# Optimization experiments

Hardware: AMD Instinct MI355X
Metric: run time of the kernel (lower is better)

Reference implementation:

```python
import jax, jax.numpy as jnp
import numpy as np

HEAD_SIZE = 64


def setup_inputs() -> dict:
    key = jax.random.key(0)
    kx, kk, kq, kv = jax.random.split(key, 4)
    B, T, C = 4, 4096, 1024
    x = jax.random.normal(kx, (B, T, C), dtype=jnp.float32)
    Wk = jax.random.normal(kk, (C, HEAD_SIZE), dtype=jnp.float32) * 0.02
    Wq = jax.random.normal(kq, (C, HEAD_SIZE), dtype=jnp.float32) * 0.02
    Wv = jax.random.normal(kv, (C, HEAD_SIZE), dtype=jnp.float32) * 0.02
    return {"x": x, "Wk": Wk, "Wq": Wq, "Wv": Wv}


def reference(x, Wk, Wq, Wv):
    # x: (B,T,C); projections to (B,T,H)
    T = x.shape[1]
    k = jnp.einsum('btc,ch->bth', x, Wk)
    q = jnp.einsum('btc,ch->bth', x, Wq)
    v = jnp.einsum('btc,ch->bth', x, Wv)
    scale = 1.0 / jnp.sqrt(jnp.float32(HEAD_SIZE))
    wei = jnp.einsum('bth,bsh->bts', q, k) * scale  # (B,T,T)
    causal = jnp.tril(jnp.ones((T, T), dtype=bool))
    wei = jnp.where(causal, wei, -jnp.inf)
    wei = jax.nn.softmax(wei, axis=-1)
    out = jnp.einsum('bts,bsh->bth', wei, v)  # (B,T,H)
    return out
```

## Files before the change

kernel.cpp:

```cpp
#include <hip/hip_runtime.h>

typedef __attribute__((ext_vector_type(8))) short short8;
typedef __attribute__((ext_vector_type(4))) float f32x4;
typedef unsigned short u16;

#define BB 4
#define TT 4096
#define CC 1024
#define HH 64

static __device__ __forceinline__ u16 f2bf(float f) {
    unsigned int u = __float_as_uint(f);
    unsigned int r = (u + 0x7FFFu + ((u >> 16) & 1u)) >> 16;
    return (u16)r;
}

static __device__ __forceinline__ unsigned int cvtpk(float lo, float hi) {
    unsigned int r;
    asm("v_cvt_pk_bf16_f32 %0, %1, %2" : "=v"(r) : "v"(lo), "v"(hi));
    return r;
}

static __device__ __forceinline__ int swz(int row, int chunk) {
    return row * 64 + ((chunk ^ (row & 7)) << 3);
}

static __device__ __forceinline__ int probe_isbf(const u16* xu, int tid) {
    int lane = tid & 63;
    int cnt = 0;
    for (int i = lane; i < 1024; i += 64) {
        u16 u = xu[2 * i];
        int e = (u >> 7) & 0xFF;
        cnt += (e >= 100 && e <= 140) ? 1 : 0;
    }
    for (int d = 1; d < 64; d <<= 1) cnt += __shfl_xor(cnt, d);
    return (cnt > 512) ? 1 : 0;
}

__global__ void prep(const void* __restrict__ Wk, const void* __restrict__ Wq,
                     const void* __restrict__ Wv, const u16* __restrict__ xu,
                     u16* __restrict__ Wtp, int* __restrict__ flag) {
    __shared__ int sflag;
    if (threadIdx.x < 64) {
        int f = probe_isbf(xu, threadIdx.x);
        if (threadIdx.x == 0) sflag = f;
    }
    __syncthreads();
    const int isbf = sflag;

    if (blockIdx.x >= 192) {
        if (threadIdx.x == 0) *flag = isbf;
        return;
    }

    int r = blockIdx.x;
    int p = r >> 6;
    int n = r & 63;
    int nt = n >> 4, nl = n & 15;
    const void* W = (p == 0) ? Wq : (p == 1) ? Wk : Wv;
    int k0 = threadIdx.x * 4;
    int kb = k0 >> 6, k2 = (k0 >> 5) & 1, quad = (k0 >> 3) & 3, half = (k0 >> 2) & 1;
    ushort4 v;
    if (isbf) {
        const u16* Wb = (const u16*)W;
        v.x = Wb[(k0 + 0) * HH + n]; v.y = Wb[(k0 + 1) * HH + n];
        v.z = Wb[(k0 + 2) * HH + n]; v.w = Wb[(k0 + 3) * HH + n];
    } else {
        const float* Wf = (const float*)W;
        v.x = f2bf(Wf[(k0 + 0) * HH + n]); v.y = f2bf(Wf[(k0 + 1) * HH + n]);
        v.z = f2bf(Wf[(k0 + 2) * HH + n]); v.w = f2bf(Wf[(k0 + 3) * HH + n]);
    }
    size_t off16 = ((size_t)((p * 4 + nt) * 16 + kb) * 2 + k2) * 64 + quad * 16 + nl;
    *reinterpret_cast<ushort4*>(Wtp + off16 * 8 + half * 4) = v;
}

__global__ __launch_bounds__(256) void qkv_proj(const void* __restrict__ x,
                                                const u16* __restrict__ Wtp,
                                                u16* __restrict__ qo, u16* __restrict__ ko,
                                                u16* __restrict__ vo, const int* __restrict__ flag) {
    __shared__ __align__(16) u16 xs[32 * 1024];
    __shared__ __align__(16) u16 tls[4][3][256];
    const int isbf = *flag;
    const int tid = threadIdx.x;
    const int lane = tid & 63;
    const int w = tid >> 6;
    const int l15 = lane & 15;
    const int quad = lane >> 4;
    int phys = blockIdx.x;
    int rb = (phys & 7) * 64 + (phys >> 3);
    const int g0r = rb * 32;

    #pragma unroll
    for (int j = 0; j < 16; j++) {
        int c = tid + j * 256;
        int row = c >> 7, ck = c & 127;
        int dst = row * 1024 + ((ck ^ (row & 7)) << 3);
        if (isbf) {
            uint4 d = *reinterpret_cast<const uint4*>((const u16*)x + (size_t)(g0r + row) * CC + ck * 8);
            *reinterpret_cast<uint4*>(xs + dst) = d;
        } else {
            const float4* pf = reinterpret_cast<const float4*>((const float*)x + (size_t)(g0r + row) * CC + ck * 8);
            float4 a0 = pf[0], a1 = pf[1];
            ushort4 lo; lo.x = f2bf(a0.x); lo.y = f2bf(a0.y); lo.z = f2bf(a0.z); lo.w = f2bf(a0.w);
            ushort4 hi; hi.x = f2bf(a1.x); hi.y = f2bf(a1.y); hi.z = f2bf(a1.z); hi.w = f2bf(a1.w);
            *reinterpret_cast<ushort4*>(xs + dst) = lo;
            *reinterpret_cast<ushort4*>(xs + dst + 4) = hi;
        }
    }
    __syncthreads();

    f32x4 zero = {0.f, 0.f, 0.f, 0.f};
    f32x4 acc[3][2];
    #pragma unroll
    for (int i = 0; i < 3; i++) { acc[i][0] = zero; acc[i][1] = zero; }

    for (int kb = 0; kb < 16; kb++) {
        #pragma unroll
        for (int k2 = 0; k2 < 2; k2++) {
            int ck = kb * 8 + k2 * 4 + quad;
            int xo = ((ck ^ (l15 & 7)) << 3);
            short8 af0 = *reinterpret_cast<const short8*>(xs + l15 * 1024 + xo);
            short8 af1 = *reinterpret_cast<const short8*>(xs + (16 + l15) * 1024 + xo);
            #pragma unroll
            for (int p = 0; p < 3; p++) {
                short8 bf = *reinterpret_cast<const short8*>(
                    Wtp + ((((size_t)(p * 4 + w) * 16 + kb) * 2 + k2) * 64 + lane) * 8);
                acc[p][0] = __builtin_amdgcn_mfma_f32_16x16x32_bf16(af0, bf, acc[p][0], 0, 0, 0);
                acc[p][1] = __builtin_amdgcn_mfma_f32_16x16x32_bf16(af1, bf, acc[p][1], 0, 0, 0);
            }
        }
    }

    const float qscale = 0.18033688011112042f;
    #pragma unroll
    for (int rt = 0; rt < 2; rt++) {
        const int g0rt = g0r + rt * 16;
        #pragma unroll
        for (int p = 0; p < 3; p++) {
            if (p < 2) {
                float sc = (p == 0) ? qscale : 1.f;
                #pragma unroll
                for (int r = 0; r < 4; r++)
                    tls[w][p][(quad * 4 + r) * 16 + l15] = f2bf(acc[p][rt][r] * sc);
            } else {
                #pragma unroll
                for (int r = 0; r < 4; r++)
                    tls[w][p][l15 * 16 + quad * 4 + r] = f2bf(acc[p][rt][r]);
            }
        }
        #pragma unroll
        for (int p = 0; p < 2; p++) {
            int t = lane >> 2, seg = lane & 3;
            ushort4 d = *reinterpret_cast<const ushort4*>(&tls[w][p][t * 16 + seg * 4]);
            u16* dst = (p == 0) ? qo : ko;
            *reinterpret_cast<ushort4*>(dst + (size_t)(g0rt + t) * HH + w * 16 + seg * 4) = d;
        }
        {
            int c = lane >> 2, seg = lane & 3;
            ushort4 d = *reinterpret_cast<const ushort4*>(&tls[w][2][c * 16 + seg * 4]);
            int b = g0rt >> 12;
            int kt = (g0rt & 4095) >> 6;
            int toff = g0rt & 63;
            *reinterpret_cast<ushort4*>(vo + ((size_t)((b * 64 + kt) * 64 + w * 16 + c)) * 64 + toff + seg * 4) = d;
        }
    }
}

__global__ __launch_bounds__(256) void attn(const u16* __restrict__ qp, const u16* __restrict__ kp,
                                            const u16* __restrict__ vp, float* __restrict__ acco,
                                            float* __restrict__ accl, void* __restrict__ outv,
                                            const int* __restrict__ flag, int nsplit) {
    __shared__ __align__(16) u16 kst[64 * 64];
    __shared__ __align__(16) u16 vts[64 * 64];
    __shared__ __align__(16) u16 pb[4][16 * 64];
    const int isbf = *flag;
    const int tid = threadIdx.x;
    const int lane = tid & 63;
    const int w = tid >> 6;
    const int l15 = lane & 15;
    const int quad = lane >> 4;

    int u = blockIdx.x;
    int b, qt, ks;
    if (nsplit == 1) {
        b = u >> 6;
        int raw = u & 63;
        qt = (raw & 1) ? (63 - (raw >> 1)) : (raw >> 1);
        ks = 0;
    } else {
        int per = 64 * nsplit;
        b = u / per;
        int rem = u - b * per;
        int i = rem / nsplit;
        qt = 63 - i;
        ks = rem - i * nsplit;
    }
    int qbase = qt * 64;
    int diag = qt;
    int nkt = diag + 1;
    if (ks >= nkt) return;

    const int q_g = qbase + w * 16 + l15;

    short8 aq[2];
    {
        const u16* qrow = qp + (size_t)(b * TT + q_g) * HH;
        aq[0] = *reinterpret_cast<const short8*>(qrow + quad * 8);
        aq[1] = *reinterpret_cast<const short8*>(qrow + 32 + quad * 8);
    }

    const int cc0 = tid, cc1 = tid + 256;
    const int dst0 = swz(cc0 >> 3, cc0 & 7);
    const int dst1 = swz(cc1 >> 3, cc1 & 7);
    const u16* kbase = kp + (size_t)b * TT * HH;
    const u16* vbase = vp + (size_t)b * 64 * 64 * 64;

    f32x4 zero = {0.f, 0.f, 0.f, 0.f};
    f32x4 o[4];
    #pragma unroll
    for (int i = 0; i < 4; i++) o[i] = zero;
    float lsum = 0.f;

    uint4 rk0 = *reinterpret_cast<const uint4*>(kbase + (size_t)ks * 4096 + cc0 * 8);
    uint4 rk1 = *reinterpret_cast<const uint4*>(kbase + (size_t)ks * 4096 + cc1 * 8);
    uint4 rv0 = *reinterpret_cast<const uint4*>(vbase + (size_t)ks * 4096 + cc0 * 8);
    uint4 rv1 = *reinterpret_cast<const uint4*>(vbase + (size_t)ks * 4096 + cc1 * 8);

    for (int kt = ks; kt < nkt; kt += nsplit) {
        __syncthreads();
        *reinterpret_cast<uint4*>(&kst[dst0]) = rk0;
        *reinterpret_cast<uint4*>(&kst[dst1]) = rk1;
        *reinterpret_cast<uint4*>(&vts[dst0]) = rv0;
        *reinterpret_cast<uint4*>(&vts[dst1]) = rv1;
        __syncthreads();
        int ktn = kt + nsplit;
        if (ktn < nkt) {
            rk0 = *reinterpret_cast<const uint4*>(kbase + (size_t)ktn * 4096 + cc0 * 8);
            rk1 = *reinterpret_cast<const uint4*>(kbase + (size_t)ktn * 4096 + cc1 * 8);
            rv0 = *reinterpret_cast<const uint4*>(vbase + (size_t)ktn * 4096 + cc0 * 8);
            rv1 = *reinterpret_cast<const uint4*>(vbase + (size_t)ktn * 4096 + cc1 * 8);
        }
        f32x4 s[4];
        #pragma unroll
        for (int i = 0; i < 4; i++) s[i] = zero;
        __builtin_amdgcn_s_setprio(1);
        #pragma unroll
        for (int k2 = 0; k2 < 2; k2++) {
            #pragma unroll
            for (int nt = 0; nt < 4; nt++) {
                short8 af = *reinterpret_cast<const short8*>(&kst[swz(nt * 16 + l15, k2 * 4 + quad)]);
                s[nt] = __builtin_amdgcn_mfma_f32_16x16x32_bf16(af, aq[k2], s[nt], 0, 0, 0);
            }
        }
        __builtin_amdgcn_s_setprio(0);
        const bool dm = (kt == diag);
        #pragma unroll
        for (int nt = 0; nt < 4; nt++) {
            int key0 = kt * 64 + nt * 16 + quad * 4;
            #pragma unroll
            for (int r = 0; r < 4; r++) {
                float p = __builtin_amdgcn_exp2f(s[nt][r]);
                if (dm && key0 + r > q_g) p = 0.f;
                s[nt][r] = p;
            }
        }
        #pragma unroll
        for (int nt = 0; nt < 4; nt++)
            lsum += (s[nt][0] + s[nt][1]) + (s[nt][2] + s[nt][3]);
        #pragma unroll
        for (int nt = 0; nt < 4; nt++) {
            uint2 pk;
            pk.x = cvtpk(s[nt][0], s[nt][1]);
            pk.y = cvtpk(s[nt][2], s[nt][3]);
            int addr = swz(l15, nt * 2 + (quad >> 1)) + (quad & 1) * 4;
            *reinterpret_cast<uint2*>(&pb[w][addr]) = pk;
        }
        __builtin_amdgcn_s_setprio(1);
        #pragma unroll
        for (int k2 = 0; k2 < 2; k2++) {
            short8 bp = *reinterpret_cast<const short8*>(&pb[w][swz(l15, k2 * 4 + quad)]);
            #pragma unroll
            for (int nt = 0; nt < 4; nt++) {
                short8 av = *reinterpret_cast<const short8*>(&vts[swz(nt * 16 + l15, k2 * 4 + quad)]);
                o[nt] = __builtin_amdgcn_mfma_f32_16x16x32_bf16(av, bp, o[nt], 0, 0, 0);
            }
        }
        __builtin_amdgcn_s_setprio(0);
    }

    lsum += __shfl_xor(lsum, 16);
    lsum += __shfl_xor(lsum, 32);

    const size_t g0q = (size_t)(b * TT) + q_g;

    if (nsplit == 1) {
        float inv = 1.0f / lsum;
        if (isbf) {
            u16* outp = (u16*)outv;
            #pragma unroll
            for (int nt = 0; nt < 4; nt++) {
                ushort4 sv;
                sv.x = f2bf(o[nt][0] * inv); sv.y = f2bf(o[nt][1] * inv);
                sv.z = f2bf(o[nt][2] * inv); sv.w = f2bf(o[nt][3] * inv);
                *reinterpret_cast<ushort4*>(outp + g0q * HH + nt * 16 + quad * 4) = sv;
            }
        } else {
            float* outp = (float*)outv;
            #pragma unroll
            for (int nt = 0; nt < 4; nt++) {
                float4 sv = {o[nt][0] * inv, o[nt][1] * inv, o[nt][2] * inv, o[nt][3] * inv};
                *reinterpret_cast<float4*>(outp + g0q * HH + nt * 16 + quad * 4) = sv;
            }
        }
    } else {
        float* accos = acco + (size_t)ks * (BB * TT * HH);
        float* accls = accl + (size_t)ks * (BB * TT);
        #pragma unroll
        for (int nt = 0; nt < 4; nt++) {
            float4 sv = {o[nt][0], o[nt][1], o[nt][2], o[nt][3]};
            *reinterpret_cast<float4*>(accos + g0q * HH + nt * 16 + quad * 4) = sv;
        }
        if (quad == 0) accls[g0q] = lsum;
    }
}

__global__ __launch_bounds__(256) void attn_finalize(const float* __restrict__ acco,
                                                     const float* __restrict__ accl,
                                                     void* __restrict__ outv,
                                                     const int* __restrict__ flag, int nsplit) {
    const int isbf = *flag;
    int i = blockIdx.x * blockDim.x + threadIdx.x;
    int row = i >> 4;
    int qt = (row & (TT - 1)) >> 6;
    int nact = min(nsplit, qt + 1);
    float4 ov = reinterpret_cast<const float4*>(acco)[i];
    float l = accl[row];
    for (int s = 1; s < nact; s++) {
        float4 t = reinterpret_cast<const float4*>(acco + (size_t)s * (BB * TT * HH))[i];
        ov.x += t.x; ov.y += t.y; ov.z += t.z; ov.w += t.w;
        l += accl[(size_t)s * (BB * TT) + row];
    }
    float inv = 1.0f / l;
    if (isbf) {
        ushort4 s;
        s.x = f2bf(ov.x * inv); s.y = f2bf(ov.y * inv);
        s.z = f2bf(ov.z * inv); s.w = f2bf(ov.w * inv);
        reinterpret_cast<ushort4*>(outv)[i] = s;
    } else {
        float4 s = {ov.x * inv, ov.y * inv, ov.z * inv, ov.w * inv};
        reinterpret_cast<float4*>(outv)[i] = s;
    }
}

extern "C" void kernel_launch(void* const* d_in, const int* in_sizes, int n_in,
                              void* d_out, int out_size, void* d_ws, size_t ws_size,
                              hipStream_t stream) {
    const void* x  = d_in[0];
    const void* Wk = d_in[1];
    const void* Wq = d_in[2];
    const void* Wv = d_in[3];
    char* ws = (char*)d_ws;
    u16* qo = (u16*)(ws);
    u16* ko = (u16*)(ws + (size_t)2 * 1024 * 1024);
    u16* vo = (u16*)(ws + (size_t)4 * 1024 * 1024);
    u16* Wtp = (u16*)(ws + (size_t)6 * 1024 * 1024);
    int* flag = (int*)(ws + (size_t)6 * 1024 * 1024 + 768 * 1024);
    float* acco = (float*)(ws + (size_t)7 * 1024 * 1024);
    float* accl = (float*)(ws + (size_t)39 * 1024 * 1024);

    const size_t need_split = (size_t)40 * 1024 * 1024;
    const int nsplit = (ws_size >= need_split) ? 8 : 1;

    prep<<<193, 256, 0, stream>>>(Wk, Wq, Wv, (const u16*)x, Wtp, flag);
    qkv_proj<<<512, 256, 0, stream>>>(x, Wtp, qo, ko, vo, flag);
    if (nsplit > 1) {
        attn<<<BB * 64 * nsplit, 256, 0, stream>>>(qo, ko, vo, acco, accl, d_out, flag, nsplit);
        attn_finalize<<<(BB * TT * HH / 4) / 256, 256, 0, stream>>>(acco, accl, d_out, flag, nsplit);
    } else {
        attn<<<BB * 64, 256, 0, stream>>>(qo, ko, vo, acco, accl, d_out, flag, 1);
    }
}
```

Before: 142.4 us.

## Pair complementary query tiles per block and double-buffer K/V LDS tiles

Each attention block now processes two query tiles (qt and 63-qt) that share every loaded K/V tile, giving balanced causal work per block and halving K/V loads per query tile. K/V shared-memory tiles are double-buffered so the next tile is staged while the current one is consumed, which removes one barrier per step. The split factor drops from 8 to 4 and the grid shrinks accordingly. This costs more LDS and registers (two accumulator sets, two Q fragments), which may lower occupancy.

```diff
diff --git a/kernel.cpp b/kernel.cpp
--- a/kernel.cpp
+++ b/kernel.cpp
@@ -166,13 +166,67 @@
     }
 }
 
+static __device__ __forceinline__ void attn_step(const u16* __restrict__ kstc,
+                                                 const u16* __restrict__ vtsc,
+                                                 u16* __restrict__ pbw,
+                                                 const short8* aq, f32x4* o, float& lsum,
+                                                 int kt, int q_g, bool dm, int l15, int quad) {
+    f32x4 zero = {0.f, 0.f, 0.f, 0.f};
+    f32x4 s[4];
+    #pragma unroll
+    for (int i = 0; i < 4; i++) s[i] = zero;
+    __builtin_amdgcn_s_setprio(1);
+    #pragma unroll
+    for (int k2 = 0; k2 < 2; k2++) {
+        #pragma unroll
+        for (int nt = 0; nt < 4; nt++) {
+            short8 af = *reinterpret_cast<const short8*>(&kstc[swz(nt * 16 + l15, k2 * 4 + quad)]);
+            s[nt] = __builtin_amdgcn_mfma_f32_16x16x32_bf16(af, aq[k2], s[nt], 0, 0, 0);
+        }
+    }
+    __builtin_amdgcn_s_setprio(0);
+    #pragma unroll
+    for (int nt = 0; nt < 4; nt++) {
+        int key0 = kt * 64 + nt * 16 + quad * 4;
+        #pragma unroll
+        for (int r = 0; r < 4; r++) {
+            float pv = __builtin_amdgcn_exp2f(s[nt][r]);
+            if (dm && key0 + r > q_g) pv = 0.f;
+            s[nt][r] = pv;
+        }
+    }
+    #pragma unroll
+    for (int nt = 0; nt < 4; nt++)
+        lsum += (s[nt][0] + s[nt][1]) + (s[nt][2] + s[nt][3]);
+    #pragma unroll
+    for (int nt = 0; nt < 4; nt++) {
+        uint2 pk;
+        pk.x = cvtpk(s[nt][0], s[nt][1]);
+        pk.y = cvtpk(s[nt][2], s[nt][3]);
+        int addr = swz(l15, nt * 2 + (quad >> 1)) + (quad & 1) * 4;
+        *reinterpret_cast<uint2*>(&pbw[addr]) = pk;
+    }
+    __builtin_amdgcn_s_setprio(1);
+    #pragma unroll
+    for (int k2 = 0; k2 < 2; k2++) {
+        short8 bp = *reinterpret_cast<const short8*>(&pbw[swz(l15, k2 * 4 + quad)]);
+        #pragma unroll
+        for (int nt = 0; nt < 4; nt++) {
+            short8 av = *reinterpret_cast<const short8*>(&vtsc[swz(nt * 16 + l15, k2 * 4 + quad)]);
+            o[nt] = __builtin_amdgcn_mfma_f32_16x16x32_bf16(av, bp, o[nt], 0, 0, 0);
+        }
+    }
+    __builtin_amdgcn_s_setprio(0);
+}
+
 __global__ __launch_bounds__(256) void attn(const u16* __restrict__ qp, const u16* __restrict__ kp,
                                             const u16* __restrict__ vp, float* __restrict__ acco,
                                             float* __restrict__ accl, void* __restrict__ outv,
                                             const int* __restrict__ flag, int nsplit) {
-    __shared__ __align__(16) u16 kst[64 * 64];
-    __shared__ __align__(16) u16 vts[64 * 64];
-    __shared__ __align__(16) u16 pb[4][16 * 64];
+    __shared__ __align__(16) u16 kst[2][64 * 64];
+    __shared__ __align__(16) u16 vts[2][64 * 64];
+    __shared__ __align__(16) u16 pba[4][16 * 64];
+    __shared__ __align__(16) u16 pbb[4][16 * 64];
     const int isbf = *flag;
     const int tid = threadIdx.x;
     const int lane = tid & 63;
@@ -181,32 +235,27 @@
     const int quad = lane >> 4;
 
     int u = blockIdx.x;
-    int b, qt, ks;
-    if (nsplit == 1) {
-        b = u >> 6;
-        int raw = u & 63;
-        qt = (raw & 1) ? (63 - (raw >> 1)) : (raw >> 1);
-        ks = 0;
-    } else {
-        int per = 64 * nsplit;
-        b = u / per;
-        int rem = u - b * per;
-        int i = rem / nsplit;
-        qt = 63 - i;
-        ks = rem - i * nsplit;
-    }
-    int qbase = qt * 64;
-    int diag = qt;
-    int nkt = diag + 1;
-    if (ks >= nkt) return;
-
-    const int q_g = qbase + w * 16 + l15;
-
-    short8 aq[2];
+    int per = 32 * nsplit;
+    int b = u / per;
+    int rem = u - b * per;
+    int p = rem / nsplit;
+    int ks = rem - p * nsplit;
+    const int qtA = 63 - p;
+    const int qtB = p;
+
+    const int q_gA = qtA * 64 + w * 16 + l15;
+    const int q_gB = qtB * 64 + w * 16 + l15;
+
+    short8 aqA[2], aqB[2];
     {
-        const u16* qrow = qp + (size_t)(b * TT + q_g) * HH;
-        aq[0] = *reinterpret_cast<const short8*>(qrow + quad * 8);
-        aq[1] = *reinterpret_cast<const short8*>(qrow + 32 + quad * 8);
+        const u16* qr = qp + (size_t)(b * TT + q_gA) * HH;
+        aqA[0] = *reinterpret_cast<const short8*>(qr + quad * 8);
+        aqA[1] = *reinterpret_cast<const short8*>(qr + 32 + quad * 8);
+    }
+    {
+        const u16* qr = qp + (size_t)(b * TT + q_gB) * HH;
+        aqB[0] = *reinterpret_cast<const short8*>(qr + quad * 8);
+        aqB[1] = *reinterpret_cast<const short8*>(qr + 32 + quad * 8);
     }
 
     const int cc0 = tid, cc1 = tid + 256;
@@ -216,100 +265,88 @@
     const u16* vbase = vp + (size_t)b * 64 * 64 * 64;
 
     f32x4 zero = {0.f, 0.f, 0.f, 0.f};
-    f32x4 o[4];
-    #pragma unroll
-    for (int i = 0; i < 4; i++) o[i] = zero;
-    float lsum = 0.f;
-
-    uint4 rk0 = *reinterpret_cast<const uint4*>(kbase + (size_t)ks * 4096 + cc0 * 8);
-    uint4 rk1 = *reinterpret_cast<const uint4*>(kbase + (size_t)ks * 4096 + cc1 * 8);
-    uint4 rv0 = *reinterpret_cast<const uint4*>(vbase + (size_t)ks * 4096 + cc0 * 8);
-    uint4 rv1 = *reinterpret_cast<const uint4*>(vbase + (size_t)ks * 4096 + cc1 * 8);
-
-    for (int kt = ks; kt < nkt; kt += nsplit) {
+    f32x4 oA[4], oB[4];
+    #pragma unroll
+    for (int i = 0; i < 4; i++) { oA[i] = zero; oB[i] = zero; }
+    float lsumA = 0.f, lsumB = 0.f;
+
+    const int nstep = (qtA - ks) / nsplit + 1;
+
+    uint4 rk0, rk1, rv0, rv1;
+    {
+        size_t t0 = (size_t)ks * 4096;
+        rk0 = *reinterpret_cast<const uint4*>(kbase + t0 + cc0 * 8);
+        rk1 = *reinterpret_cast<const uint4*>(kbase + t0 + cc1 * 8);
+        rv0 = *reinterpret_cast<const uint4*>(vbase + t0 + cc0 * 8);
+        rv1 = *reinterpret_cast<const uint4*>(vbase + t0 + cc1 * 8);
+    }
+    *reinterpret_cast<uint4*>(&kst[0][dst0]) = rk0;
+    *reinterpret_cast<uint4*>(&kst[0][dst1]) = rk1;
+    *reinterpret_cast<uint4*>(&vts[0][dst0]) = rv0;
+    *reinterpret_cast<uint4*>(&vts[0][dst1]) = rv1;
+    if (nstep > 1) {
+        size_t t1 = (size_t)(ks + nsplit) * 4096;
+        rk0 = *reinterpret_cast<const uint4*>(kbase + t1 + cc0 * 8);
+        rk1 = *reinterpret_cast<const uint4*>(kbase + t1 + cc1 * 8);
+        rv0 = *reinterpret_cast<const uint4*>(vbase + t1 + cc0 * 8);
+        rv1 = *reinterpret_cast<const uint4*>(vbase + t1 + cc1 * 8);
+    }
+
+    for (int j = 0; j < nstep; ++j) {
         __syncthreads();
-        *reinterpret_cast<uint4*>(&kst[dst0]) = rk0;
-        *reinterpret_cast<uint4*>(&kst[dst1]) = rk1;
-        *reinterpret_cast<uint4*>(&vts[dst0]) = rv0;
-        *reinterpret_cast<uint4*>(&vts[dst1]) = rv1;
-        __syncthreads();
-        int ktn = kt + nsplit;
-        if (ktn < nkt) {
-            rk0 = *reinterpret_cast<const uint4*>(kbase + (size_t)ktn * 4096 + cc0 * 8);
-            rk1 = *reinterpret_cast<const uint4*>(kbase + (size_t)ktn * 4096 + cc1 * 8);
-            rv0 = *reinterpret_cast<const uint4*>(vbase + (size_t)ktn * 4096 + cc0 * 8);
-            rv1 = *reinterpret_cast<const uint4*>(vbase + (size_t)ktn * 4096 + cc1 * 8);
-        }
-        f32x4 s[4];
-        #pragma unroll
-        for (int i = 0; i < 4; i++) s[i] = zero;
-        __builtin_amdgcn_s_setprio(1);
-        #pragma unroll
-        for (int k2 = 0; k2 < 2; k2++) {
-            #pragma unroll
-            for (int nt = 0; nt < 4; nt++) {
-                short8 af = *reinterpret_cast<const short8*>(&kst[swz(nt * 16 + l15, k2 * 4 + quad)]);
-                s[nt] = __builtin_amdgcn_mfma_f32_16x16x32_bf16(af, aq[k2], s[nt], 0, 0, 0);
-            }
-        }
-        __builtin_amdgcn_s_setprio(0);
-        const bool dm = (kt == diag);
-        #pragma unroll
-        for (int nt = 0; nt < 4; nt++) {
-            int key0 = kt * 64 + nt * 16 + quad * 4;
-            #pragma unroll
-            for (int r = 0; r < 4; r++) {
-                float p = __builtin_amdgcn_exp2f(s[nt][r]);
-                if (dm && key0 + r > q_g) p = 0.f;
-                s[nt][r] = p;
-            }
-        }
-        #pragma unroll
-        for (int nt = 0; nt < 4; nt++)
-            lsum += (s[nt][0] + s[nt][1]) + (s[nt][2] + s[nt][3]);
-        #pragma unroll
-        for (int nt = 0; nt < 4; nt++) {
-            uint2 pk;
-            pk.x = cvtpk(s[nt][0], s[nt][1]);
-            pk.y = cvtpk(s[nt][2], s[nt][3]);
-            int addr = swz(l15, nt * 2 + (quad >> 1)) + (quad & 1) * 4;
-            *reinterpret_cast<uint2*>(&pb[w][addr]) = pk;
-        }
-        __builtin_amdgcn_s_setprio(1);
-        #pragma unroll
-        for (int k2 = 0; k2 < 2; k2++) {
-            short8 bp = *reinterpret_cast<const short8*>(&pb[w][swz(l15, k2 * 4 + quad)]);
-            #pragma unroll
-            for (int nt = 0; nt < 4; nt++) {
-                short8 av = *reinterpret_cast<const short8*>(&vts[swz(nt * 16 + l15, k2 * 4 + quad)]);
-                o[nt] = __builtin_amdgcn_mfma_f32_16x16x32_bf16(av, bp, o[nt], 0, 0, 0);
-            }
-        }
-        __builtin_amdgcn_s_setprio(0);
-    }
-
-    lsum += __shfl_xor(lsum, 16);
-    lsum += __shfl_xor(lsum, 32);
-
-    const size_t g0q = (size_t)(b * TT) + q_g;
+        const int cur = j & 1;
+        if (j + 1 < nstep) {
+            *reinterpret_cast<uint4*>(&kst[cur ^ 1][dst0]) = rk0;
+            *reinterpret_cast<uint4*>(&kst[cur ^ 1][dst1]) = rk1;
+            *reinterpret_cast<uint4*>(&vts[cur ^ 1][dst0]) = rv0;
+            *reinterpret_cast<uint4*>(&vts[cur ^ 1][dst1]) = rv1;
+        }
+        if (j + 2 < nstep) {
+            size_t tn = (size_t)(ks + (j + 2) * nsplit) * 4096;
+            rk0 = *reinterpret_cast<const uint4*>(kbase + tn + cc0 * 8);
+            rk1 = *reinterpret_cast<const uint4*>(kbase + tn + cc1 * 8);
+            rv0 = *reinterpret_cast<const uint4*>(vbase + tn + cc0 * 8);
+            rv1 = *reinterpret_cast<const uint4*>(vbase + tn + cc1 * 8);
+        }
+        const int kt = ks + j * nsplit;
+        attn_step(&kst[cur][0], &vts[cur][0], &pba[w][0], aqA, oA, lsumA,
+                  kt, q_gA, kt == qtA, l15, quad);
+        if (kt <= qtB)
+            attn_step(&kst[cur][0], &vts[cur][0], &pbb[w][0], aqB, oB, lsumB,
+                      kt, q_gB, kt == qtB, l15, quad);
+    }
+
+    lsumA += __shfl_xor(lsumA, 16);
+    lsumA += __shfl_xor(lsumA, 32);
+    lsumB += __shfl_xor(lsumB, 16);
+    lsumB += __shfl_xor(lsumB, 32);
+
+    const size_t g0qA = (size_t)(b * TT) + q_gA;
+    const size_t g0qB = (size_t)(b * TT) + q_gB;
 
     if (nsplit == 1) {
-        float inv = 1.0f / lsum;
+        float invA = 1.0f / lsumA;
+        float invB = 1.0f / lsumB;
         if (isbf) {
             u16* outp = (u16*)outv;
             #pragma unroll
             for (int nt = 0; nt < 4; nt++) {
-                ushort4 sv;
-                sv.x = f2bf(o[nt][0] * inv); sv.y = f2bf(o[nt][1] * inv);
-                sv.z = f2bf(o[nt][2] * inv); sv.w = f2bf(o[nt][3] * inv);
-                *reinterpret_cast<ushort4*>(outp + g0q * HH + nt * 16 + quad * 4) = sv;
+                ushort4 sa, sb;
+                sa.x = f2bf(oA[nt][0] * invA); sa.y = f2bf(oA[nt][1] * invA);
+                sa.z = f2bf(oA[nt][2] * invA); sa.w = f2bf(oA[nt][3] * invA);
+                sb.x = f2bf(oB[nt][0] * invB); sb.y = f2bf(oB[nt][1] * invB);
+                sb.z = f2bf(oB[nt][2] * invB); sb.w = f2bf(oB[nt][3] * invB);
+                *reinterpret_cast<ushort4*>(outp + g0qA * HH + nt * 16 + quad * 4) = sa;
+                *reinterpret_cast<ushort4*>(outp + g0qB * HH + nt * 16 + quad * 4) = sb;
             }
         } else {
             float* outp = (float*)outv;
             #pragma unroll
             for (int nt = 0; nt < 4; nt++) {
-                float4 sv = {o[nt][0] * inv, o[nt][1] * inv, o[nt][2] * inv, o[nt][3] * inv};
-                *reinterpret_cast<float4*>(outp + g0q * HH + nt * 16 + quad * 4) = sv;
+                float4 sa = {oA[nt][0] * invA, oA[nt][1] * invA, oA[nt][2] * invA, oA[nt][3] * invA};
+                float4 sb = {oB[nt][0] * invB, oB[nt][1] * invB, oB[nt][2] * invB, oB[nt][3] * invB};
+                *reinterpret_cast<float4*>(outp + g0qA * HH + nt * 16 + quad * 4) = sa;
+                *reinterpret_cast<float4*>(outp + g0qB * HH + nt * 16 + quad * 4) = sb;
             }
         }
     } else {
@@ -317,10 +354,18 @@
         float* accls = accl + (size_t)ks * (BB * TT);
         #pragma unroll
         for (int nt = 0; nt < 4; nt++) {
-            float4 sv = {o[nt][0], o[nt][1], o[nt][2], o[nt][3]};
-            *reinterpret_cast<float4*>(accos + g0q * HH + nt * 16 + quad * 4) = sv;
-        }
-        if (quad == 0) accls[g0q] = lsum;
+            float4 sv = {oA[nt][0], oA[nt][1], oA[nt][2], oA[nt][3]};
+            *reinterpret_cast<float4*>(accos + g0qA * HH + nt * 16 + quad * 4) = sv;
+        }
+        if (quad == 0) accls[g0qA] = lsumA;
+        if (ks <= qtB) {
+            #pragma unroll
+            for (int nt = 0; nt < 4; nt++) {
+                float4 sv = {oB[nt][0], oB[nt][1], oB[nt][2], oB[nt][3]};
+                *reinterpret_cast<float4*>(accos + g0qB * HH + nt * 16 + quad * 4) = sv;
+            }
+            if (quad == 0) accls[g0qB] = lsumB;
+        }
     }
 }
 
@@ -369,14 +414,12 @@
     float* accl = (float*)(ws + (size_t)39 * 1024 * 1024);
 
     const size_t need_split = (size_t)40 * 1024 * 1024;
-    const int nsplit = (ws_size >= need_split) ? 8 : 1;
+    const int nsplit = (ws_size >= need_split) ? 4 : 1;
 
     prep<<<193, 256, 0, stream>>>(Wk, Wq, Wv, (const u16*)x, Wtp, flag);
     qkv_proj<<<512, 256, 0, stream>>>(x, Wtp, qo, ko, vo, flag);
+    attn<<<BB * 32 * nsplit, 256, 0, stream>>>(qo, ko, vo, acco, accl, d_out, flag, nsplit);
     if (nsplit > 1) {
-        attn<<<BB * 64 * nsplit, 256, 0, stream>>>(qo, ko, vo, acco, accl, d_out, flag, nsplit);
         attn_finalize<<<(BB * TT * HH / 4) / 256, 256, 0, stream>>>(acco, accl, d_out, flag, nsplit);
-    } else {
-        attn<<<BB * 64, 256, 0, stream>>>(qo, ko, vo, acco, accl, d_out, flag, 1);
-    }
-}
+    }
+}
```

Result: no change. 139.8 us (-1.8%).
